# Performance work log

Hardware: AMD Instinct MI355X
Metric: run time of the kernel (lower is better)

## Reference

```python
import jax, jax.numpy as jnp
from jax import lax
import numpy as np

D_IN, D_MODEL, N_CLS, NL = 63, 256, 14, 4
D_INNER, D_STATE, NH, HP, DCONV = 512, 128, 8, 64, 4
CONV_CH = D_INNER + 2 * D_STATE  # 768
PROJ = 2 * D_INNER + 2 * D_STATE + NH  # 1288
EPS = 1e-5


def layernorm(x, w, b):
    mu = jnp.mean(x, -1, keepdims=True)
    var = jnp.mean((x - mu) ** 2, -1, keepdims=True)
    return (x - mu) * lax.rsqrt(var + EPS) * w + b


def mamba2_block(u, inproj_w, conv_w, conv_b, dt_bias, A_log, Dp, norm_w, outp_w):
    B, L, _ = u.shape
    zxbcdt = u @ inproj_w.T  # (B,L,1288)
    z = zxbcdt[..., :D_INNER]
    xBC = zxbcdt[..., D_INNER:D_INNER + CONV_CH]
    dt = zxbcdt[..., D_INNER + CONV_CH:]  # (B,L,NH)
    # depthwise causal conv1d, kernel 4
    xp = jnp.pad(xBC, ((0, 0), (DCONV - 1, 0), (0, 0)))
    conv = conv_b + sum(xp[:, k:k + L, :] * conv_w[k] for k in range(DCONV))
    xBC = jax.nn.silu(conv)
    xs = xBC[..., :D_INNER].reshape(B, L, NH, HP)
    Bm = xBC[..., D_INNER:D_INNER + D_STATE]  # (B,L,N)
    Cm = xBC[..., D_INNER + D_STATE:]
    dt = jax.nn.softplus(dt + dt_bias)  # (B,L,NH)
    A = -jnp.exp(A_log)  # (NH,)
    dA = jnp.exp(dt * A)  # (B,L,NH)
    dtx = dt[..., None] * xs  # (B,L,NH,HP)

    def step(h, inp):
        dA_t, dtx_t, B_t, C_t = inp
        h = h * dA_t[:, :, None, None] + jnp.einsum('bhp,bn->bhpn', dtx_t, B_t)
        y = jnp.einsum('bhpn,bn->bhp', h, C_t)
        return h, y

    h0 = jnp.zeros((B, NH, HP, D_STATE), u.dtype)
    _, ys = lax.scan(step, h0, (dA.transpose(1, 0, 2), dtx.transpose(1, 0, 2, 3),
                                 Bm.transpose(1, 0, 2), Cm.transpose(1, 0, 2)))
    y = ys.transpose(1, 0, 2, 3) + Dp[None, None, :, None] * xs  # (B,L,NH,HP)
    y = y.reshape(B, L, D_INNER)
    g = y * jax.nn.silu(z)  # gated RMSNorm (norm_before_gate=False)
    g = g * lax.rsqrt(jnp.mean(g * g, -1, keepdims=True) + EPS) * norm_w
    return g @ outp_w.T


def setup_inputs() -> dict:
    key = jax.random.key(0)
    ks = jax.random.split(key, 20)
    B, L = 32, 1024
    s = 0.02
    inp = {
        'x': jax.random.normal(ks[0], (B, L, D_IN), jnp.float32),
        'in_w': jax.random.normal(ks[1], (D_MODEL, D_IN)) * s,
        'in_b': jnp.zeros((D_MODEL,)),
        'lnin_w': jnp.ones((D_MODEL,)),
        'lnin_b': jnp.zeros((D_MODEL,)),
        'inproj_w': jax.random.normal(ks[2], (NL, PROJ, D_MODEL)) * s,
        'conv_w': jax.random.normal(ks[3], (NL, DCONV, CONV_CH)) * 0.1,
        'conv_b': jnp.zeros((NL, CONV_CH)),
        'dt_bias': jax.random.uniform(ks[4], (NL, NH), minval=-4.0, maxval=-1.0),
        'A_log': jnp.log(jax.random.uniform(ks[5], (NL, NH), minval=1.0, maxval=16.0)),
        'D': jnp.ones((NL, NH)),
        'norm_w': jnp.ones((NL, D_INNER)),
        'outp_w': jax.random.normal(ks[6], (NL, D_MODEL, D_INNER)) * s,
        'ln_w': jnp.ones((NL, D_MODEL)),
        'ln_b': jnp.zeros((NL, D_MODEL)),
        'head_w': jax.random.normal(ks[7], (N_CLS, D_MODEL)) * s,
        'head_b': jnp.zeros((N_CLS,)),
        'lengths': jax.random.randint(ks[8], (B,), 1, L + 1, dtype=jnp.int32),
    }
    return inp


def reference(x, in_w, in_b, lnin_w, lnin_b, inproj_w, conv_w, conv_b, dt_bias,
              A_log, D, norm_w, outp_w, ln_w, ln_b, head_w, head_b, lengths):
    B, L, _ = x.shape
    h = layernorm(x @ in_w.T + in_b, lnin_w, lnin_b)
    for i in range(NL):
        res = h
        m = mamba2_block(h, inproj_w[i], conv_w[i], conv_b[i], dt_bias[i],
                         A_log[i], D[i], norm_w[i], outp_w[i])
        h = layernorm(m + res, ln_w[i], ln_b[i])
    mask = (jnp.arange(L)[None, :] < lengths[:, None]).astype(h.dtype)[:, :, None]
    pooled = jnp.sum(h * mask, axis=1) / lengths[:, None].astype(h.dtype)
    return pooled @ head_w.T + head_b
```

## Files before the change

### kernel.cpp

```cpp
#include <hip/hip_runtime.h>
#include <math.h>

#define D_IN 63
#define D_MODEL 256
#define N_CLS 14
#define NL 4
#define D_INNER 512
#define D_STATE 128
#define NH 8
#define HP 64
#define DCONV 4
#define CONV_CH 768
#define PROJ 1288
#define XBCDT 776
#define EPS 1e-5f
#define BSZ 32
#define LSEQ 1024
#define NTOK (BSZ*LSEQ)

#define SSEG 4
#define TSEG (LSEQ/SSEG)
#define CT 16
#define RS 8

#define S_IN   16384
#define S_IP   1318912
#define S_OP   524288
#define IN_HI  0
#define IN_LO  16384
#define IP_HI  32768
#define IP_LO  (32768 + S_IP)
#define OP_HI  (32768 + 2*S_IP)
#define OP_LO  (OP_HI + S_OP)
#define TOTPK  (S_IN + S_IP + S_OP)
#define WS_BASE ((size_t)NTOK * 1816)
#define WS_NEED ((WS_BASE + (size_t)TOTPK) * 4)

typedef __attribute__((ext_vector_type(8))) short bf16x8;
typedef __attribute__((ext_vector_type(4))) float f32x4;

__device__ __forceinline__ float silu_f(float x) { return x / (1.f + expf(-x)); }

__device__ __forceinline__ unsigned short f2bf(float x) {
    union { float f; unsigned u; } v; v.f = x;
    unsigned r = v.u + 0x7FFFu + ((v.u >> 16) & 1u);
    return (unsigned short)(r >> 16);
}
__device__ __forceinline__ float bf2f(unsigned short h) {
    union { float f; unsigned u; } v; v.u = ((unsigned)h) << 16; return v.f;
}

__device__ __forceinline__ int swz128(int n) {
    int q = n >> 5, i = (n >> 2) & 7, j = n & 3;
    return (q << 5) + (((i + 2 * q) & 7) << 2) + j;
}

__device__ __forceinline__ float2 block_reduce2(float a, float b, float* sred) {
    #pragma unroll
    for (int off = 32; off >= 1; off >>= 1) {
        a += __shfl_xor(a, off);
        b += __shfl_xor(b, off);
    }
    int wid = threadIdx.x >> 6, lane = threadIdx.x & 63;
    if (lane == 0) { sred[wid * 2] = a; sred[wid * 2 + 1] = b; }
    __syncthreads();
    a = sred[0] + sred[2] + sred[4] + sred[6];
    b = sred[1] + sred[3] + sred[5] + sred[7];
    __syncthreads();
    return make_float2(a, b);
}

__global__ __launch_bounds__(256)
void k_pack_weights(const float* __restrict__ in_w, const float* __restrict__ inproj,
                    const float* __restrict__ outp, unsigned short* __restrict__ WP) {
    int idx = blockIdx.x * 256 + threadIdx.x;
    float v; int hi_off, lo_off;
    if (idx < S_IN) {
        int n = idx >> 6, k = idx & 63;
        v = (k < D_IN) ? in_w[n * D_IN + k] : 0.f;
        hi_off = IN_HI + idx; lo_off = IN_LO + idx;
    } else if (idx < S_IN + S_IP) {
        int j = idx - S_IN;
        v = inproj[j];
        hi_off = IP_HI + j; lo_off = IP_LO + j;
    } else {
        int j = idx - S_IN - S_IP;
        v = outp[j];
        hi_off = OP_HI + j; lo_off = OP_LO + j;
    }
    unsigned short h = f2bf(v);
    unsigned short l = f2bf(v - bf2f(h));
    WP[hi_off] = h; WP[lo_off] = l;
}

#define LDKP 40
__global__ __launch_bounds__(256, 2)
void k_gemm_as(const float* __restrict__ A, const unsigned short* __restrict__ Bhg,
               const unsigned short* __restrict__ Blg, float* __restrict__ C,
               int M, int N, int K) {
    __shared__ unsigned short Ah[128][LDKP], Al[128][LDKP];
    __shared__ unsigned short Bh[128][LDKP], Bl[128][LDKP];
    int n0 = blockIdx.x * 128, m0 = blockIdx.y * 128;
    int tid = threadIdx.x;
    int srow = tid >> 1, sk = (tid & 1) * 16;
    int lane = tid & 63, wave = tid >> 6;
    int wm = (wave >> 1) * 64, wn = (wave & 1) * 64;
    int ln = lane & 15, quad = lane >> 4;
    f32x4 acc[4][4];
    #pragma unroll
    for (int i = 0; i < 4; i++)
        #pragma unroll
        for (int j = 0; j < 4; j++) acc[i][j] = (f32x4){0.f, 0.f, 0.f, 0.f};
    const float* Ap = A + (size_t)(m0 + srow) * K + sk;
    const unsigned short* Bhp = Bhg + (size_t)(n0 + srow) * K + sk;
    const unsigned short* Blp = Blg + (size_t)(n0 + srow) * K + sk;
    bool bval = (n0 + srow) < N;
    uint4 z4 = make_uint4(0u, 0u, 0u, 0u);
    for (int k0 = 0; k0 < K; k0 += 32) {
        float av[16];
        #pragma unroll
        for (int i = 0; i < 4; i++)
            *(float4*)&av[4 * i] = *(const float4*)(Ap + k0 + 4 * i);
        uint4 bh0 = bval ? *(const uint4*)(Bhp + k0) : z4;
        uint4 bh1 = bval ? *(const uint4*)(Bhp + k0 + 8) : z4;
        uint4 bl0 = bval ? *(const uint4*)(Blp + k0) : z4;
        uint4 bl1 = bval ? *(const uint4*)(Blp + k0 + 8) : z4;
        unsigned hp[8], lp[8];
        #pragma unroll
        for (int j = 0; j < 8; j++) {
            float a0 = av[2 * j], a1 = av[2 * j + 1];
            unsigned u0 = __float_as_uint(a0), u1 = __float_as_uint(a1);
            unsigned h0 = u0 & 0xFFFF0000u, h1 = u1 & 0xFFFF0000u;
            float r0 = a0 - __uint_as_float(h0);
            float r1 = a1 - __uint_as_float(h1);
            hp[j] = (u0 >> 16) | h1;
            lp[j] = (__float_as_uint(r0) >> 16) | (__float_as_uint(r1) & 0xFFFF0000u);
        }
        __syncthreads();
        *(uint4*)&Ah[srow][sk]     = *(uint4*)&hp[0];
        *(uint4*)&Ah[srow][sk + 8] = *(uint4*)&hp[4];
        *(uint4*)&Al[srow][sk]     = *(uint4*)&lp[0];
        *(uint4*)&Al[srow][sk + 8] = *(uint4*)&lp[4];
        *(uint4*)&Bh[srow][sk]     = bh0;
        *(uint4*)&Bh[srow][sk + 8] = bh1;
        *(uint4*)&Bl[srow][sk]     = bl0;
        *(uint4*)&Bl[srow][sk + 8] = bl1;
        __syncthreads();
        bf16x8 fah[4], fal[4], fbh[4], fbl[4];
        #pragma unroll
        for (int t = 0; t < 4; t++) {
            fah[t] = *(const bf16x8*)&Ah[wm + t * 16 + ln][quad * 8];
            fal[t] = *(const bf16x8*)&Al[wm + t * 16 + ln][quad * 8];
            fbh[t] = *(const bf16x8*)&Bh[wn + t * 16 + ln][quad * 8];
            fbl[t] = *(const bf16x8*)&Bl[wn + t * 16 + ln][quad * 8];
        }
        #pragma unroll
        for (int mt = 0; mt < 4; mt++)
            #pragma unroll
            for (int nt = 0; nt < 4; nt++) {
                acc[mt][nt] = __builtin_amdgcn_mfma_f32_16x16x32_bf16(fal[mt], fbh[nt], acc[mt][nt], 0, 0, 0);
                acc[mt][nt] = __builtin_amdgcn_mfma_f32_16x16x32_bf16(fah[mt], fbl[nt], acc[mt][nt], 0, 0, 0);
                acc[mt][nt] = __builtin_amdgcn_mfma_f32_16x16x32_bf16(fah[mt], fbh[nt], acc[mt][nt], 0, 0, 0);
            }
    }
    #pragma unroll
    for (int mt = 0; mt < 4; mt++)
        #pragma unroll
        for (int nt = 0; nt < 4; nt++) {
            int cn = n0 + wn + nt * 16 + ln;
            if (cn < N) {
                #pragma unroll
                for (int r = 0; r < 4; r++) {
                    int cm = m0 + wm + mt * 16 + quad * 4 + r;
                    C[(size_t)cm * N + cn] = acc[mt][nt][r];
                }
            }
        }
}

__global__ __launch_bounds__(256, 2)
void k_gemm_mfma(const float* __restrict__ A, const float* __restrict__ B,
                 float* __restrict__ C, int M, int N, int K) {
    __shared__ unsigned short Ah[128][LDKP], Al[128][LDKP];
    __shared__ unsigned short Bh[128][LDKP], Bl[128][LDKP];
    int n0 = blockIdx.x * 128, m0 = blockIdx.y * 128;
    int tid = threadIdx.x;
    int srow = tid >> 1, sk = (tid & 1) * 16;
    int lane = tid & 63, wave = tid >> 6;
    int wm = (wave >> 1) * 64, wn = (wave & 1) * 64;
    int ln = lane & 15, quad = lane >> 4;
    f32x4 acc[4][4];
    #pragma unroll
    for (int i = 0; i < 4; i++)
        #pragma unroll
        for (int j = 0; j < 4; j++) acc[i][j] = (f32x4){0.f, 0.f, 0.f, 0.f};
    const float* Ap = A + (size_t)(m0 + srow) * K + sk;
    const float* Bp = B + (size_t)(n0 + srow) * K + sk;
    bool bval = (n0 + srow) < N;
    for (int k0 = 0; k0 < K; k0 += 32) {
        float av[16], bv[16];
        #pragma unroll
        for (int i = 0; i < 4; i++) {
            *(float4*)&av[4 * i] = *(const float4*)(Ap + k0 + 4 * i);
            *(float4*)&bv[4 * i] = bval ? *(const float4*)(Bp + k0 + 4 * i)
                                        : make_float4(0.f, 0.f, 0.f, 0.f);
        }
        __syncthreads();
        #pragma unroll
        for (int g = 0; g < 2; g++) {
            unsigned hiA[4], loA[4], hiB[4], loB[4];
            #pragma unroll
            for (int j = 0; j < 4; j++) {
                float a0 = av[8 * g + 2 * j], a1 = av[8 * g + 2 * j + 1];
                unsigned short h0 = f2bf(a0), h1 = f2bf(a1);
                unsigned short l0 = f2bf(a0 - bf2f(h0)), l1 = f2bf(a1 - bf2f(h1));
                hiA[j] = (unsigned)h0 | ((unsigned)h1 << 16);
                loA[j] = (unsigned)l0 | ((unsigned)l1 << 16);
                float b0 = bv[8 * g + 2 * j], b1 = bv[8 * g + 2 * j + 1];
                unsigned short g0 = f2bf(b0), g1 = f2bf(b1);
                unsigned short m0s = f2bf(b0 - bf2f(g0)), m1s = f2bf(b1 - bf2f(g1));
                hiB[j] = (unsigned)g0 | ((unsigned)g1 << 16);
                loB[j] = (unsigned)m0s | ((unsigned)m1s << 16);
            }
            *(uint4*)&Ah[srow][sk + 8 * g] = *(uint4*)hiA;
            *(uint4*)&Al[srow][sk + 8 * g] = *(uint4*)loA;
            *(uint4*)&Bh[srow][sk + 8 * g] = *(uint4*)hiB;
            *(uint4*)&Bl[srow][sk + 8 * g] = *(uint4*)loB;
        }
        __syncthreads();
        bf16x8 fah[4], fal[4], fbh[4], fbl[4];
        #pragma unroll
        for (int t = 0; t < 4; t++) {
            fah[t] = *(const bf16x8*)&Ah[wm + t * 16 + ln][quad * 8];
            fal[t] = *(const bf16x8*)&Al[wm + t * 16 + ln][quad * 8];
            fbh[t] = *(const bf16x8*)&Bh[wn + t * 16 + ln][quad * 8];
            fbl[t] = *(const bf16x8*)&Bl[wn + t * 16 + ln][quad * 8];
        }
        #pragma unroll
        for (int mt = 0; mt < 4; mt++)
            #pragma unroll
            for (int nt = 0; nt < 4; nt++) {
                acc[mt][nt] = __builtin_amdgcn_mfma_f32_16x16x32_bf16(fal[mt], fbh[nt], acc[mt][nt], 0, 0, 0);
                acc[mt][nt] = __builtin_amdgcn_mfma_f32_16x16x32_bf16(fah[mt], fbl[nt], acc[mt][nt], 0, 0, 0);
                acc[mt][nt] = __builtin_amdgcn_mfma_f32_16x16x32_bf16(fah[mt], fbh[nt], acc[mt][nt], 0, 0, 0);
            }
    }
    #pragma unroll
    for (int mt = 0; mt < 4; mt++)
        #pragma unroll
        for (int nt = 0; nt < 4; nt++) {
            int cn = n0 + wn + nt * 16 + ln;
            if (cn < N) {
                #pragma unroll
                for (int r = 0; r < 4; r++) {
                    int cm = m0 + wm + mt * 16 + quad * 4 + r;
                    C[(size_t)cm * N + cn] = acc[mt][nt][r];
                }
            }
        }
}

__global__ __launch_bounds__(256)
void k_pack_x(const float* __restrict__ x, float* __restrict__ xp) {
    size_t idx = (size_t)blockIdx.x * 256 + threadIdx.x;
    int k = (int)(idx & 63);
    size_t m = idx >> 6;
    xp[idx] = (k < D_IN) ? x[m * D_IN + k] : 0.f;
}
__global__ __launch_bounds__(256)
void k_pack_w(const float* __restrict__ w, float* __restrict__ wp) {
    int idx = blockIdx.x * 256 + threadIdx.x;
    int k = idx & 63, n = idx >> 6;
    wp[idx] = (k < D_IN) ? w[n * D_IN + k] : 0.f;
}

__global__ __launch_bounds__(256)
void k_lnio(const float* __restrict__ pre, const float* __restrict__ bias,
            const float* __restrict__ gw, const float* __restrict__ gb,
            float* __restrict__ h) {
    int m = blockIdx.x, o = threadIdx.x;
    __shared__ float sred[8];
    float v = pre[(size_t)m * D_MODEL + o] + bias[o];
    float2 s = block_reduce2(v, v * v, sred);
    float mu = s.x * (1.f / D_MODEL);
    float var = s.y * (1.f / D_MODEL) - mu * mu;
    h[(size_t)m * D_MODEL + o] = (v - mu) * rsqrtf(var + EPS) * gw[o] + gb[o];
}

__global__ __launch_bounds__(256)
void k_conv(const float* __restrict__ xbc, const float* __restrict__ cw,
            const float* __restrict__ cb, const float* __restrict__ dtb,
            float* __restrict__ xs, float* __restrict__ Bm, float* __restrict__ Cm,
            float* __restrict__ dtv) {
    int m = blockIdx.x;
    int l = m & (LSEQ - 1);
    int tid = threadIdx.x;
    #pragma unroll
    for (int it = 0; it < 3; it++) {
        int c = tid + it * 256;
        float acc = cb[c];
        #pragma unroll
        for (int k = 0; k < DCONV; k++) {
            int lp = l - (DCONV - 1) + k;
            if (lp >= 0)
                acc = fmaf(cw[k * CONV_CH + c],
                           xbc[(size_t)(m - (DCONV - 1) + k) * XBCDT + c], acc);
        }
        float v = silu_f(acc);
        if (c < D_INNER) xs[(size_t)m * D_INNER + c] = v;
        else if (c < D_INNER + D_STATE) Bm[(size_t)m * D_STATE + (c - D_INNER)] = v;
        else Cm[(size_t)m * D_STATE + (c - D_INNER - D_STATE)] = v;
    }
    if (tid < NH) {
        float draw = xbc[(size_t)m * XBCDT + CONV_CH + tid] + dtb[tid];
        float dt = draw > 20.f ? draw : log1pf(expf(draw));
        dtv[m * NH + tid] = dt;
    }
}

__global__ __launch_bounds__(256, 4)
void k_scan_seg(const float* __restrict__ xs, const float* __restrict__ Bm,
                const float* __restrict__ Cm, const float* __restrict__ dtv,
                const float* __restrict__ Alog, const float* __restrict__ Dvec,
                float* __restrict__ y, float* __restrict__ F,
                float* __restrict__ cumdA) {
    int blk = blockIdx.x;
    int bh = blk >> 2;
    int seg = blk & (SSEG - 1);
    int b = bh >> 3, hh = bh & 7;
    int tid = threadIdx.x;
    int p = tid >> 2, q = tid & 3;
    int q2 = q << 1;
    __shared__ __align__(16) float sBC[2 * CT * 128];
    __shared__ __align__(16) float sX[CT][HP];
    __shared__ float sdt[CT], sdA[CT], srdA[CT];
    float hst[32];
    #pragma unroll
    for (int i = 0; i < 32; i++) hst[i] = 0.f;
    float Dh = Dvec[hh];
    float Ahv = -expf(Alog[hh]);
    float c_run = 1.f;
    const size_t base = (size_t)b * LSEQ + (size_t)seg * TSEG;
    int col = tid & 127, half = tid >> 7;
    int sw = swz128(col);
    int xc = tid & 63, xh = tid >> 6;

    for (int c0 = 0; c0 < TSEG; c0 += CT) {
        #pragma unroll
        for (int u = 0; u < 8; u++) {
            int s = 2 * u + half;
            size_t m = base + c0 + s;
            sBC[s * 128 + sw] = Bm[m * D_STATE + col];
            sBC[(CT + s) * 128 + sw] = Cm[m * D_STATE + col];
        }
        #pragma unroll
        for (int u = 0; u < 4; u++) {
            int s = 4 * u + xh;
            sX[s][xc] = xs[(base + c0 + s) * D_INNER + hh * HP + xc];
        }
        if (tid < CT) {
            float dtl = dtv[(base + c0 + tid) * NH + hh];
            float e = fmaxf(dtl * Ahv, -37.f);
            sdt[tid] = dtl;
            sdA[tid] = expf(e);
            srdA[tid] = expf(-e);
        }
        __syncthreads();
        if (tid == 0) {
            float cg = c_run;
            for (int s = 0; s < CT; s++) {
                cg *= sdA[s];
                cumdA[(base + c0 + s) * NH + hh] = cg;
            }
            c_run = cg;
        }
        float cc = 1.f, rc = 1.f;
        #pragma unroll
        for (int s = 0; s < CT; s++) {
            float dAl = sdA[s], dtl = sdt[s];
            float ccn = cc * dAl;
            if (ccn < 1e-18f) {
                #pragma unroll
                for (int i = 0; i < 32; i++) hst[i] *= cc;
                rc = srdA[s];
                ccn = dAl;
            } else {
                rc *= srdA[s];
            }
            cc = ccn;
            float xv = sX[s][p];
            float tmp = dtl * xv * rc;
            float yp = 0.f;
            #pragma unroll
            for (int i = 0; i < 8; i++) {
                int off = (q << 5) + (((i + q2) & 7) << 2);
                float4 bv = *(const float4*)&sBC[s * 128 + off];
                float4 cv = *(const float4*)&sBC[(CT + s) * 128 + off];
                hst[4*i+0] = fmaf(tmp, bv.x, hst[4*i+0]); yp = fmaf(hst[4*i+0], cv.x, yp);
                hst[4*i+1] = fmaf(tmp, bv.y, hst[4*i+1]); yp = fmaf(hst[4*i+1], cv.y, yp);
                hst[4*i+2] = fmaf(tmp, bv.z, hst[4*i+2]); yp = fmaf(hst[4*i+2], cv.z, yp);
                hst[4*i+3] = fmaf(tmp, bv.w, hst[4*i+3]); yp = fmaf(hst[4*i+3], cv.w, yp);
            }
            yp += __shfl_xor(yp, 1);
            yp += __shfl_xor(yp, 2);
            if (q == 0) y[(base + c0 + s) * D_INNER + hh * HP + p] = fmaf(Dh, xv, cc * yp);
            if ((s & (RS - 1)) == RS - 1) {
                #pragma unroll
                for (int i = 0; i < 32; i++) hst[i] *= cc;
                cc = 1.f; rc = 1.f;
            }
        }
        __syncthreads();
    }
    if (seg < SSEG - 1) {
        float* Fp = F + (((size_t)bh * (SSEG - 1) + seg) * HP + p) * D_STATE + (q << 5);
        #pragma unroll
        for (int i = 0; i < 8; i++)
            *(float4*)(Fp + 4 * i) = make_float4(hst[4*i], hst[4*i+1], hst[4*i+2], hst[4*i+3]);
    }
}

__global__ __launch_bounds__(256, 4)
void k_seg_fix(const float* __restrict__ Cm, const float* __restrict__ cumdA,
               const float* __restrict__ F, float* __restrict__ y) {
    int blk = blockIdx.x;
    int bh = blk / (SSEG - 1);
    int seg = blk - bh * (SSEG - 1) + 1;
    int b = bh >> 3, hh = bh & 7;
    int tid = threadIdx.x, p = tid >> 2, q = tid & 3;
    int q2 = q << 1;
    float hin[32];
    #pragma unroll
    for (int i = 0; i < 32; i++) hin[i] = 0.f;
    for (int s = 0; s < seg; s++) {
        float P = cumdA[((size_t)b * LSEQ + (size_t)(s + 1) * TSEG - 1) * NH + hh];
        const float* Fp = F + (((size_t)bh * (SSEG - 1) + s) * HP + p) * D_STATE + (q << 5);
        #pragma unroll
        for (int i = 0; i < 8; i++) {
            float4 f = *(const float4*)(Fp + 4 * i);
            hin[4*i+0] = fmaf(hin[4*i+0], P, f.x);
            hin[4*i+1] = fmaf(hin[4*i+1], P, f.y);
            hin[4*i+2] = fmaf(hin[4*i+2], P, f.z);
            hin[4*i+3] = fmaf(hin[4*i+3], P, f.w);
        }
    }
    __shared__ __align__(16) float sC[CT][D_STATE];
    __shared__ float scd[CT];
    const size_t base = (size_t)b * LSEQ + (size_t)seg * TSEG;
    int col = tid & 127, half = tid >> 7;
    int sw = swz128(col);
    for (int c0 = 0; c0 < TSEG; c0 += CT) {
        #pragma unroll
        for (int u = 0; u < 8; u++) {
            int s = 2 * u + half;
            sC[s][sw] = Cm[(base + c0 + s) * D_STATE + col];
        }
        if (tid < CT) scd[tid] = cumdA[(base + c0 + tid) * NH + hh];
        __syncthreads();
        #pragma unroll 1
        for (int s = 0; s < CT; s++) {
            float yp = 0.f;
            #pragma unroll
            for (int i = 0; i < 8; i++) {
                int off = (q << 5) + (((i + q2) & 7) << 2);
                float4 cvv = *(const float4*)&sC[s][off];
                yp = fmaf(hin[4*i+0], cvv.x, yp);
                yp = fmaf(hin[4*i+1], cvv.y, yp);
                yp = fmaf(hin[4*i+2], cvv.z, yp);
                yp = fmaf(hin[4*i+3], cvv.w, yp);
            }
            yp += __shfl_xor(yp, 1);
            yp += __shfl_xor(yp, 2);
            if (q == 0) {
                size_t idx = (base + c0 + s) * D_INNER + hh * HP + p;
                y[idx] += scd[s] * yp;
            }
        }
        __syncthreads();
    }
}

__global__ __launch_bounds__(256)
void k_gate(float* __restrict__ y, const float* __restrict__ zbuf,
            const float* __restrict__ nw) {
    int m = blockIdx.x, tid = threadIdx.x;
    __shared__ float sred[8];
    float g[2];
    #pragma unroll
    for (int j = 0; j < 2; j++) {
        int d = tid + j * 256;
        float z = zbuf[(size_t)m * D_INNER + d];
        g[j] = y[(size_t)m * D_INNER + d] * silu_f(z);
    }
    float2 s = block_reduce2(g[0] * g[0] + g[1] * g[1], 0.f, sred);
    float r = rsqrtf(s.x * (1.f / D_INNER) + EPS);
    #pragma unroll
    for (int j = 0; j < 2; j++) {
        int d = tid + j * 256;
        y[(size_t)m * D_INNER + d] = g[j] * r * nw[d];
    }
}

__global__ __launch_bounds__(256)
void k_addln(const float* __restrict__ mo, float* __restrict__ h,
             const float* __restrict__ w, const float* __restrict__ bias) {
    int m = blockIdx.x, o = threadIdx.x;
    __shared__ float sred[8];
    float v = mo[(size_t)m * D_MODEL + o] + h[(size_t)m * D_MODEL + o];
    float2 s = block_reduce2(v, v * v, sred);
    float mu = s.x * (1.f / D_MODEL);
    float var = s.y * (1.f / D_MODEL) - mu * mu;
    h[(size_t)m * D_MODEL + o] = (v - mu) * rsqrtf(var + EPS) * w[o] + bias[o];
}

__global__ __launch_bounds__(256)
void k_pool_head(const float* __restrict__ h, const int* __restrict__ len,
                 const float* __restrict__ hw, const float* __restrict__ hb,
                 float* __restrict__ out) {
    int b = blockIdx.x, d = threadIdx.x;
    __shared__ float sp[D_MODEL];
    int Lb = len[b];
    float acc = 0.f;
    for (int l = 0; l < Lb; l++) acc += h[((size_t)b * LSEQ + l) * D_MODEL + d];
    sp[d] = acc / (float)Lb;
    __syncthreads();
    if (d < N_CLS) {
        float o = hb[d];
        const float* wr = hw + (size_t)d * D_MODEL;
        #pragma unroll 8
        for (int k = 0; k < D_MODEL; k++) o = fmaf(sp[k], wr[k], o);
        out[b * N_CLS + d] = o;
    }
}

extern "C" void kernel_launch(void* const* d_in, const int* in_sizes, int n_in,
                              void* d_out, int out_size, void* d_ws, size_t ws_size,
                              hipStream_t stream) {
    const float* x      = (const float*)d_in[0];
    const float* in_w   = (const float*)d_in[1];
    const float* in_b   = (const float*)d_in[2];
    const float* lnin_w = (const float*)d_in[3];
    const float* lnin_b = (const float*)d_in[4];
    const float* inproj = (const float*)d_in[5];
    const float* conv_w = (const float*)d_in[6];
    const float* conv_b = (const float*)d_in[7];
    const float* dt_bias= (const float*)d_in[8];
    const float* A_log  = (const float*)d_in[9];
    const float* Dv     = (const float*)d_in[10];
    const float* norm_w = (const float*)d_in[11];
    const float* outp_w = (const float*)d_in[12];
    const float* ln_w   = (const float*)d_in[13];
    const float* ln_b   = (const float*)d_in[14];
    const float* head_w = (const float*)d_in[15];
    const float* head_b = (const float*)d_in[16];
    const int*   lengths= (const int*)d_in[17];
    float* out = (float*)d_out;

    float* ws    = (float*)d_ws;
    float* h     = ws;
    float* buf1  = h    + (size_t)NTOK * D_MODEL;
    float* xs    = buf1 + (size_t)NTOK * XBCDT;
    float* Bm    = xs   + (size_t)NTOK * D_INNER;
    float* Cm    = Bm   + (size_t)NTOK * D_STATE;
    float* dtv   = Cm   + (size_t)NTOK * D_STATE;
    float* cumdA = dtv  + (size_t)NTOK * NH;
    float* zbuf  = buf1;
    float* F     = buf1 + (size_t)NTOK * D_INNER;
    float* mo    = Bm;
    float* xp    = buf1;
    float* pre   = buf1 + (size_t)NTOK * 64;
    unsigned short* WP = (unsigned short*)(ws + WS_BASE);
    bool use_pk = (ws_size >= WS_NEED);

    dim3 gIO(D_MODEL / 128, NTOK / 128);
    dim3 g1a((XBCDT + 127) / 128, NTOK / 128);
    dim3 g1b(D_INNER / 128, NTOK / 128);

    if (use_pk) {
        k_pack_weights<<<TOTPK / 256, 256, 0, stream>>>(in_w, inproj, outp_w, WP);
        k_pack_x<<<NTOK * 64 / 256, 256, 0, stream>>>(x, xp);
        k_gemm_as<<<gIO, 256, 0, stream>>>(xp, WP + IN_HI, WP + IN_LO, pre,
                                           NTOK, D_MODEL, 64);
        k_lnio<<<NTOK, 256, 0, stream>>>(pre, in_b, lnin_w, lnin_b, h);
        for (int i = 0; i < NL; i++) {
            const unsigned short* iph = WP + IP_HI + (size_t)i * PROJ * D_MODEL;
            const unsigned short* ipl = WP + IP_LO + (size_t)i * PROJ * D_MODEL;
            k_gemm_as<<<g1a, 256, 0, stream>>>(h, iph + (size_t)D_INNER * D_MODEL,
                                               ipl + (size_t)D_INNER * D_MODEL,
                                               buf1, NTOK, XBCDT, D_MODEL);
            k_conv<<<NTOK, 256, 0, stream>>>(buf1, conv_w + i * DCONV * CONV_CH,
                                             conv_b + i * CONV_CH, dt_bias + i * NH,
                                             xs, Bm, Cm, dtv);
            k_gemm_as<<<g1b, 256, 0, stream>>>(h, iph, ipl, zbuf, NTOK, D_INNER, D_MODEL);
            k_scan_seg<<<BSZ * NH * SSEG, 256, 0, stream>>>(xs, Bm, Cm, dtv,
                                                            A_log + i * NH, Dv + i * NH,
                                                            xs, F, cumdA);
            k_seg_fix<<<BSZ * NH * (SSEG - 1), 256, 0, stream>>>(Cm, cumdA, F, xs);
            k_gate<<<NTOK, 256, 0, stream>>>(xs, zbuf, norm_w + i * D_INNER);
            k_gemm_as<<<gIO, 256, 0, stream>>>(xs, WP + OP_HI + (size_t)i * D_MODEL * D_INNER,
                                               WP + OP_LO + (size_t)i * D_MODEL * D_INNER,
                                               mo, NTOK, D_MODEL, D_INNER);
            k_addln<<<NTOK, 256, 0, stream>>>(mo, h, ln_w + i * D_MODEL, ln_b + i * D_MODEL);
        }
    } else {
        float* wp = Bm;
        k_pack_x<<<NTOK * 64 / 256, 256, 0, stream>>>(x, xp);
        k_pack_w<<<64, 256, 0, stream>>>(in_w, wp);
        k_gemm_mfma<<<gIO, 256, 0, stream>>>(xp, wp, pre, NTOK, D_MODEL, 64);
        k_lnio<<<NTOK, 256, 0, stream>>>(pre, in_b, lnin_w, lnin_b, h);
        for (int i = 0; i < NL; i++) {
            const float* W = inproj + (size_t)i * PROJ * D_MODEL;
            k_gemm_mfma<<<g1a, 256, 0, stream>>>(h, W + (size_t)D_INNER * D_MODEL,
                                                 buf1, NTOK, XBCDT, D_MODEL);
            k_conv<<<NTOK, 256, 0, stream>>>(buf1, conv_w + i * DCONV * CONV_CH,
                                             conv_b + i * CONV_CH, dt_bias + i * NH,
                                             xs, Bm, Cm, dtv);
            k_gemm_mfma<<<g1b, 256, 0, stream>>>(h, W, zbuf, NTOK, D_INNER, D_MODEL);
            k_scan_seg<<<BSZ * NH * SSEG, 256, 0, stream>>>(xs, Bm, Cm, dtv,
                                                            A_log + i * NH, Dv + i * NH,
                                                            xs, F, cumdA);
            k_seg_fix<<<BSZ * NH * (SSEG - 1), 256, 0, stream>>>(Cm, cumdA, F, xs);
            k_gate<<<NTOK, 256, 0, stream>>>(xs, zbuf, norm_w + i * D_INNER);
            k_gemm_mfma<<<gIO, 256, 0, stream>>>(xs, outp_w + (size_t)i * D_MODEL * D_INNER,
                                                 mo, NTOK, D_MODEL, D_INNER);
            k_addln<<<NTOK, 256, 0, stream>>>(mo, h, ln_w + i * D_MODEL, ln_b + i * D_MODEL);
        }
    }

    k_pool_head<<<BSZ, 256, 0, stream>>>(h, lengths, head_w, head_b, out);
}
```

Baseline: 3.014 ms.

## Split scan head dimension across two blocks and parallelize pooling over sequence chunks

The selective-scan and segment-fix kernels now split each head's 64 channels across two blocks. Each thread keeps 16 state values instead of 32, with 8 lanes per channel, a shorter 8-step chunk and renormalization once per chunk. This doubles the grid and halves register pressure (launch bounds raised to 8 blocks per SM) to raise occupancy on the latency-bound recurrence, at the cost of loading B/C twice and an extra shuffle. The final masked mean-pool is also split into 16 sequence chunks per batch followed by a small head kernel, replacing a 32-block serial loop over up to 1024 tokens.

Result: no change. 3.011 ms (-0.1%).

```diff
diff --git a/kernel.cpp b/kernel.cpp
--- a/kernel.cpp
+++ b/kernel.cpp
@@ -20,8 +20,7 @@
 
 #define SSEG 4
 #define TSEG (LSEQ/SSEG)
-#define CT 16
-#define RS 8
+#define CTS 8
 
 #define S_IN   16384
 #define S_IP   1318912
@@ -50,9 +49,9 @@
     union { float f; unsigned u; } v; v.u = ((unsigned)h) << 16; return v.f;
 }
 
-__device__ __forceinline__ int swz128(int n) {
-    int q = n >> 5, i = (n >> 2) & 7, j = n & 3;
-    return (q << 5) + (((i + 2 * q) & 7) << 2) + j;
+__device__ __forceinline__ int swz8(int n) {
+    int g = n >> 4, j = (n >> 2) & 3, e = n & 3;
+    return (g << 4) + (((j + (g >> 1)) & 3) << 2) + e;
 }
 
 __device__ __forceinline__ float2 block_reduce2(float a, float b, float* sred) {
@@ -318,47 +317,46 @@
     }
 }
 
-__global__ __launch_bounds__(256, 4)
+__global__ __launch_bounds__(256, 8)
 void k_scan_seg(const float* __restrict__ xs, const float* __restrict__ Bm,
                 const float* __restrict__ Cm, const float* __restrict__ dtv,
                 const float* __restrict__ Alog, const float* __restrict__ Dvec,
                 float* __restrict__ y, float* __restrict__ F,
                 float* __restrict__ cumdA) {
     int blk = blockIdx.x;
-    int bh = blk >> 2;
-    int seg = blk & (SSEG - 1);
+    int pb  = blk & 1;
+    int seg = (blk >> 1) & (SSEG - 1);
+    int bh  = blk >> 3;
     int b = bh >> 3, hh = bh & 7;
     int tid = threadIdx.x;
-    int p = tid >> 2, q = tid & 3;
-    int q2 = q << 1;
-    __shared__ __align__(16) float sBC[2 * CT * 128];
-    __shared__ __align__(16) float sX[CT][HP];
-    __shared__ float sdt[CT], sdA[CT], srdA[CT];
-    float hst[32];
-    #pragma unroll
-    for (int i = 0; i < 32; i++) hst[i] = 0.f;
+    int q = tid & 7;
+    int pl = tid >> 3;
+    int p = pl + pb * 32;
+    __shared__ __align__(16) float sBC[2 * CTS * 128];
+    __shared__ __align__(16) float sX[CTS][32];
+    __shared__ float sdt[CTS], sdA[CTS], srdA[CTS];
+    float hst[16];
+    #pragma unroll
+    for (int i = 0; i < 16; i++) hst[i] = 0.f;
     float Dh = Dvec[hh];
     float Ahv = -expf(Alog[hh]);
     float c_run = 1.f;
     const size_t base = (size_t)b * LSEQ + (size_t)seg * TSEG;
     int col = tid & 127, half = tid >> 7;
-    int sw = swz128(col);
-    int xc = tid & 63, xh = tid >> 6;
-
-    for (int c0 = 0; c0 < TSEG; c0 += CT) {
-        #pragma unroll
-        for (int u = 0; u < 8; u++) {
+    int sw = swz8(col);
+    int xc = tid & 31, xh = tid >> 5;
+    int q2 = q >> 1;
+
+    for (int c0 = 0; c0 < TSEG; c0 += CTS) {
+        #pragma unroll
+        for (int u = 0; u < 4; u++) {
             int s = 2 * u + half;
             size_t m = base + c0 + s;
             sBC[s * 128 + sw] = Bm[m * D_STATE + col];
-            sBC[(CT + s) * 128 + sw] = Cm[m * D_STATE + col];
-        }
-        #pragma unroll
-        for (int u = 0; u < 4; u++) {
-            int s = 4 * u + xh;
-            sX[s][xc] = xs[(base + c0 + s) * D_INNER + hh * HP + xc];
-        }
-        if (tid < CT) {
+            sBC[(CTS + s) * 128 + sw] = Cm[m * D_STATE + col];
+        }
+        sX[xh][xc] = xs[(base + c0 + xh) * D_INNER + hh * HP + pb * 32 + xc];
+        if (tid < CTS) {
             float dtl = dtv[(base + c0 + tid) * NH + hh];
             float e = fmaxf(dtl * Ahv, -37.f);
             sdt[tid] = dtl;
@@ -366,36 +364,38 @@
             srdA[tid] = expf(-e);
         }
         __syncthreads();
-        if (tid == 0) {
+        if (pb == 0 && tid == 0) {
             float cg = c_run;
-            for (int s = 0; s < CT; s++) {
+            for (int s = 0; s < CTS; s++) {
                 cg *= sdA[s];
                 cumdA[(base + c0 + s) * NH + hh] = cg;
             }
             c_run = cg;
+        } else if (tid == 0) {
+            for (int s = 0; s < CTS; s++) c_run *= sdA[s];
         }
         float cc = 1.f, rc = 1.f;
         #pragma unroll
-        for (int s = 0; s < CT; s++) {
+        for (int s = 0; s < CTS; s++) {
             float dAl = sdA[s], dtl = sdt[s];
             float ccn = cc * dAl;
             if (ccn < 1e-18f) {
                 #pragma unroll
-                for (int i = 0; i < 32; i++) hst[i] *= cc;
+                for (int i = 0; i < 16; i++) hst[i] *= cc;
                 rc = srdA[s];
                 ccn = dAl;
             } else {
                 rc *= srdA[s];
             }
             cc = ccn;
-            float xv = sX[s][p];
+            float xv = sX[s][pl];
             float tmp = dtl * xv * rc;
             float yp = 0.f;
             #pragma unroll
-            for (int i = 0; i < 8; i++) {
-                int off = (q << 5) + (((i + q2) & 7) << 2);
+            for (int i = 0; i < 4; i++) {
+                int off = (q << 4) + (((i + q2) & 3) << 2);
                 float4 bv = *(const float4*)&sBC[s * 128 + off];
-                float4 cv = *(const float4*)&sBC[(CT + s) * 128 + off];
+                float4 cv = *(const float4*)&sBC[(CTS + s) * 128 + off];
                 hst[4*i+0] = fmaf(tmp, bv.x, hst[4*i+0]); yp = fmaf(hst[4*i+0], cv.x, yp);
                 hst[4*i+1] = fmaf(tmp, bv.y, hst[4*i+1]); yp = fmaf(hst[4*i+1], cv.y, yp);
                 hst[4*i+2] = fmaf(tmp, bv.z, hst[4*i+2]); yp = fmaf(hst[4*i+2], cv.z, yp);
@@ -403,40 +403,45 @@
             }
             yp += __shfl_xor(yp, 1);
             yp += __shfl_xor(yp, 2);
+            yp += __shfl_xor(yp, 4);
             if (q == 0) y[(base + c0 + s) * D_INNER + hh * HP + p] = fmaf(Dh, xv, cc * yp);
-            if ((s & (RS - 1)) == RS - 1) {
+            if (s == CTS - 1) {
                 #pragma unroll
-                for (int i = 0; i < 32; i++) hst[i] *= cc;
-                cc = 1.f; rc = 1.f;
+                for (int i = 0; i < 16; i++) hst[i] *= cc;
             }
         }
         __syncthreads();
     }
     if (seg < SSEG - 1) {
-        float* Fp = F + (((size_t)bh * (SSEG - 1) + seg) * HP + p) * D_STATE + (q << 5);
-        #pragma unroll
-        for (int i = 0; i < 8; i++)
+        float* Fp = F + (((size_t)bh * (SSEG - 1) + seg) * HP + p) * D_STATE + (q << 4);
+        #pragma unroll
+        for (int i = 0; i < 4; i++)
             *(float4*)(Fp + 4 * i) = make_float4(hst[4*i], hst[4*i+1], hst[4*i+2], hst[4*i+3]);
     }
 }
 
-__global__ __launch_bounds__(256, 4)
+__global__ __launch_bounds__(256, 8)
 void k_seg_fix(const float* __restrict__ Cm, const float* __restrict__ cumdA,
                const float* __restrict__ F, float* __restrict__ y) {
     int blk = blockIdx.x;
-    int bh = blk / (SSEG - 1);
-    int seg = blk - bh * (SSEG - 1) + 1;
+    int pb = blk & 1;
+    int t2 = blk >> 1;
+    int bh = t2 / (SSEG - 1);
+    int seg = t2 - bh * (SSEG - 1) + 1;
     int b = bh >> 3, hh = bh & 7;
-    int tid = threadIdx.x, p = tid >> 2, q = tid & 3;
-    int q2 = q << 1;
-    float hin[32];
-    #pragma unroll
-    for (int i = 0; i < 32; i++) hin[i] = 0.f;
+    int tid = threadIdx.x;
+    int q = tid & 7;
+    int pl = tid >> 3;
+    int p = pl + pb * 32;
+    int q2 = q >> 1;
+    float hin[16];
+    #pragma unroll
+    for (int i = 0; i < 16; i++) hin[i] = 0.f;
     for (int s = 0; s < seg; s++) {
         float P = cumdA[((size_t)b * LSEQ + (size_t)(s + 1) * TSEG - 1) * NH + hh];
-        const float* Fp = F + (((size_t)bh * (SSEG - 1) + s) * HP + p) * D_STATE + (q << 5);
-        #pragma unroll
-        for (int i = 0; i < 8; i++) {
+        const float* Fp = F + (((size_t)bh * (SSEG - 1) + s) * HP + p) * D_STATE + (q << 4);
+        #pragma unroll
+        for (int i = 0; i < 4; i++) {
             float4 f = *(const float4*)(Fp + 4 * i);
             hin[4*i+0] = fmaf(hin[4*i+0], P, f.x);
             hin[4*i+1] = fmaf(hin[4*i+1], P, f.y);
@@ -444,33 +449,34 @@
             hin[4*i+3] = fmaf(hin[4*i+3], P, f.w);
         }
     }
-    __shared__ __align__(16) float sC[CT][D_STATE];
-    __shared__ float scd[CT];
+    __shared__ __align__(16) float sC[CTS * 128];
+    __shared__ float scd[CTS];
     const size_t base = (size_t)b * LSEQ + (size_t)seg * TSEG;
     int col = tid & 127, half = tid >> 7;
-    int sw = swz128(col);
-    for (int c0 = 0; c0 < TSEG; c0 += CT) {
-        #pragma unroll
-        for (int u = 0; u < 8; u++) {
+    int sw = swz8(col);
+    for (int c0 = 0; c0 < TSEG; c0 += CTS) {
+        #pragma unroll
+        for (int u = 0; u < 4; u++) {
             int s = 2 * u + half;
-            sC[s][sw] = Cm[(base + c0 + s) * D_STATE + col];
-        }
-        if (tid < CT) scd[tid] = cumdA[(base + c0 + tid) * NH + hh];
-        __syncthreads();
-        #pragma unroll 1
-        for (int s = 0; s < CT; s++) {
+            sC[s * 128 + sw] = Cm[(base + c0 + s) * D_STATE + col];
+        }
+        if (tid < CTS) scd[tid] = cumdA[(base + c0 + tid) * NH + hh];
+        __syncthreads();
+        #pragma unroll
+        for (int s = 0; s < CTS; s++) {
             float yp = 0.f;
             #pragma unroll
-            for (int i = 0; i < 8; i++) {
-                int off = (q << 5) + (((i + q2) & 7) << 2);
-                float4 cvv = *(const float4*)&sC[s][off];
-                yp = fmaf(hin[4*i+0], cvv.x, yp);
-                yp = fmaf(hin[4*i+1], cvv.y, yp);
-                yp = fmaf(hin[4*i+2], cvv.z, yp);
-                yp = fmaf(hin[4*i+3], cvv.w, yp);
+            for (int i = 0; i < 4; i++) {
+                int off = (q << 4) + (((i + q2) & 3) << 2);
+                float4 cv = *(const float4*)&sC[s * 128 + off];
+                yp = fmaf(hin[4*i+0], cv.x, yp);
+                yp = fmaf(hin[4*i+1], cv.y, yp);
+                yp = fmaf(hin[4*i+2], cv.z, yp);
+                yp = fmaf(hin[4*i+3], cv.w, yp);
             }
             yp += __shfl_xor(yp, 1);
             yp += __shfl_xor(yp, 2);
+            yp += __shfl_xor(yp, 4);
             if (q == 0) {
                 size_t idx = (base + c0 + s) * D_INNER + hh * HP + p;
                 y[idx] += scd[s] * yp;
@@ -514,15 +520,29 @@
 }
 
 __global__ __launch_bounds__(256)
-void k_pool_head(const float* __restrict__ h, const int* __restrict__ len,
-                 const float* __restrict__ hw, const float* __restrict__ hb,
-                 float* __restrict__ out) {
+void k_pool_part(const float* __restrict__ h, const int* __restrict__ len,
+                 float* __restrict__ part) {
+    int blk = blockIdx.x;
+    int b = blk >> 4, ch = blk & 15;
+    int d = threadIdx.x;
+    int Lb = len[b];
+    int l0 = ch * 64;
+    int le = min(l0 + 64, Lb);
+    float acc = 0.f;
+    for (int l = l0; l < le; l++) acc += h[((size_t)b * LSEQ + l) * D_MODEL + d];
+    part[(size_t)blk * D_MODEL + d] = acc;
+}
+
+__global__ __launch_bounds__(256)
+void k_head(const float* __restrict__ part, const int* __restrict__ len,
+            const float* __restrict__ hw, const float* __restrict__ hb,
+            float* __restrict__ out) {
     int b = blockIdx.x, d = threadIdx.x;
     __shared__ float sp[D_MODEL];
-    int Lb = len[b];
-    float acc = 0.f;
-    for (int l = 0; l < Lb; l++) acc += h[((size_t)b * LSEQ + l) * D_MODEL + d];
-    sp[d] = acc / (float)Lb;
+    float a = 0.f;
+    #pragma unroll
+    for (int c = 0; c < 16; c++) a += part[(size_t)(b * 16 + c) * D_MODEL + d];
+    sp[d] = a / (float)len[b];
     __syncthreads();
     if (d < N_CLS) {
         float o = hb[d];
@@ -569,12 +589,15 @@
     float* mo    = Bm;
     float* xp    = buf1;
     float* pre   = buf1 + (size_t)NTOK * 64;
+    float* poolp = buf1;
     unsigned short* WP = (unsigned short*)(ws + WS_BASE);
     bool use_pk = (ws_size >= WS_NEED);
 
     dim3 gIO(D_MODEL / 128, NTOK / 128);
     dim3 g1a((XBCDT + 127) / 128, NTOK / 128);
     dim3 g1b(D_INNER / 128, NTOK / 128);
+    int gScan = BSZ * NH * SSEG * 2;
+    int gFix  = BSZ * NH * (SSEG - 1) * 2;
 
     if (use_pk) {
         k_pack_weights<<<TOTPK / 256, 256, 0, stream>>>(in_w, inproj, outp_w, WP);
@@ -592,10 +615,10 @@
                                              conv_b + i * CONV_CH, dt_bias + i * NH,
                                              xs, Bm, Cm, dtv);
             k_gemm_as<<<g1b, 256, 0, stream>>>(h, iph, ipl, zbuf, NTOK, D_INNER, D_MODEL);
-            k_scan_seg<<<BSZ * NH * SSEG, 256, 0, stream>>>(xs, Bm, Cm, dtv,
-                                                            A_log + i * NH, Dv + i * NH,
-                                                            xs, F, cumdA);
-            k_seg_fix<<<BSZ * NH * (SSEG - 1), 256, 0, stream>>>(Cm, cumdA, F, xs);
+            k_scan_seg<<<gScan, 256, 0, stream>>>(xs, Bm, Cm, dtv,
+                                                  A_log + i * NH, Dv + i * NH,
+                                                  xs, F, cumdA);
+            k_seg_fix<<<gFix, 256, 0, stream>>>(Cm, cumdA, F, xs);
             k_gate<<<NTOK, 256, 0, stream>>>(xs, zbuf, norm_w + i * D_INNER);
             k_gemm_as<<<gIO, 256, 0, stream>>>(xs, WP + OP_HI + (size_t)i * D_MODEL * D_INNER,
                                                WP + OP_LO + (size_t)i * D_MODEL * D_INNER,
@@ -616,10 +639,10 @@
                                              conv_b + i * CONV_CH, dt_bias + i * NH,
                                              xs, Bm, Cm, dtv);
             k_gemm_mfma<<<g1b, 256, 0, stream>>>(h, W, zbuf, NTOK, D_INNER, D_MODEL);
-            k_scan_seg<<<BSZ * NH * SSEG, 256, 0, stream>>>(xs, Bm, Cm, dtv,
-                                                            A_log + i * NH, Dv + i * NH,
-                                                            xs, F, cumdA);
-            k_seg_fix<<<BSZ * NH * (SSEG - 1), 256, 0, stream>>>(Cm, cumdA, F, xs);
+            k_scan_seg<<<gScan, 256, 0, stream>>>(xs, Bm, Cm, dtv,
+                                                  A_log + i * NH, Dv + i * NH,
+                                                  xs, F, cumdA);
+            k_seg_fix<<<gFix, 256, 0, stream>>>(Cm, cumdA, F, xs);
             k_gate<<<NTOK, 256, 0, stream>>>(xs, zbuf, norm_w + i * D_INNER);
             k_gemm_mfma<<<gIO, 256, 0, stream>>>(xs, outp_w + (size_t)i * D_MODEL * D_INNER,
                                                  mo, NTOK, D_MODEL, D_INNER);
@@ -627,5 +650,6 @@
         }
     }
 
-    k_pool_head<<<BSZ, 256, 0, stream>>>(h, lengths, head_w, head_b, out);
-}
+    k_pool_part<<<BSZ * 16, 256, 0, stream>>>(h, lengths, poolp);
+    k_head<<<BSZ, 256, 0, stream>>>(poolp, lengths, head_w, head_b, out);
+}
```
